# Performance work log

Hardware: AMD Instinct MI355X
Metric: run time of the kernel (lower is better)

Reference implementation:

```python
import jax, jax.numpy as jnp
import numpy as np

LOG_MAX = float(np.log(1000.0 / 16.0))  # dw/dh clamp from BoxCoder.decode
NMS_THRESH = 0.7


def setup_inputs() -> dict:
    key = jax.random.key(0)
    k1, k2, k3, k4, k5, k6 = jax.random.split(key, 6)
    N, B = 262144, 4
    im_h, im_w = 800, 1280
    # plausible anchors: random centers inside image, sizes in [16, 216]
    cx = jax.random.uniform(k1, (N,)) * im_w
    cy = jax.random.uniform(k2, (N,)) * im_h
    aw = jax.random.uniform(k3, (N,)) * 200.0 + 16.0
    ah = jax.random.uniform(k4, (N,)) * 200.0 + 16.0
    anchors = jnp.stack([cx - 0.5 * aw, cy - 0.5 * ah, cx + 0.5 * aw, cy + 0.5 * ah], axis=1).astype(jnp.float32)
    pred_bbox_deltas = (jax.random.normal(k5, (B, N, 4)) * 0.2).astype(jnp.float32)
    objectness = jax.random.normal(k6, (B, N)).astype(jnp.float32)
    return {
        'anchors': anchors,
        'pred_bbox_deltas': pred_bbox_deltas,
        'objectness': objectness,
        'im_h': im_h,
        'im_w': im_w,
        'post_nms_top_n': 1000,
    }


def _decode_clip(anchors, deltas, im_h, im_w):
    # BoxCoder.decode with weights (1,1,1,1), then clip to image bounds.
    aw = anchors[:, 2] - anchors[:, 0]          # [N]
    ah = anchors[:, 3] - anchors[:, 1]
    acx = anchors[:, 0] + 0.5 * aw
    acy = anchors[:, 1] + 0.5 * ah
    dx, dy = deltas[..., 0], deltas[..., 1]     # [B,N]
    dw = jnp.minimum(deltas[..., 2], LOG_MAX)
    dh = jnp.minimum(deltas[..., 3], LOG_MAX)
    pcx = dx * aw + acx
    pcy = dy * ah + acy
    pw = jnp.exp(dw) * aw
    ph = jnp.exp(dh) * ah
    x1 = jnp.clip(pcx - 0.5 * pw, 0.0, im_w)
    y1 = jnp.clip(pcy - 0.5 * ph, 0.0, im_h)
    x2 = jnp.clip(pcx + 0.5 * pw, 0.0, im_w)
    y2 = jnp.clip(pcy + 0.5 * ph, 0.0, im_h)
    return jnp.stack([x1, y1, x2, y2], axis=-1)  # [B,N,4]


def _nms_indices(boxes, scores, k):
    # Greedy NMS (torchvision semantics: suppress IoU > thresh), fixed k picks.
    bs = jax.lax.stop_gradient(boxes)           # indices are non-differentiable
    ss = jax.lax.stop_gradient(scores)
    areas = (bs[:, 2] - bs[:, 0]) * (bs[:, 3] - bs[:, 1])

    def body(cur, _):
        i = jnp.argmax(cur)
        picked = cur[i]
        bb = bs[i]
        ix1 = jnp.maximum(bb[0], bs[:, 0])
        iy1 = jnp.maximum(bb[1], bs[:, 1])
        ix2 = jnp.minimum(bb[2], bs[:, 2])
        iy2 = jnp.minimum(bb[3], bs[:, 3])
        inter = jnp.maximum(ix2 - ix1, 0.0) * jnp.maximum(iy2 - iy1, 0.0)
        barea = (bb[2] - bb[0]) * (bb[3] - bb[1])
        iou = inter / (barea + areas - inter + 1e-9)
        cur = jnp.where(iou > NMS_THRESH, -jnp.inf, cur).at[i].set(-jnp.inf)
        return cur, (i, picked)

    _, (idx, picked) = jax.lax.scan(body, ss, None, length=k)
    return idx, jnp.isfinite(picked)            # valid flags pad positions


def reference(anchors, pred_bbox_deltas, objectness, im_h, im_w, post_nms_top_n):
    boxes = _decode_clip(anchors, pred_bbox_deltas, float(im_h), float(im_w))  # [B,N,4]
    area = (boxes[..., 2] - boxes[..., 0]) * (boxes[..., 3] - boxes[..., 1])
    # area > 1 filter, expressed as score masking (keeps shapes static)
    scores = jnp.where(area > 1.0, objectness, -jnp.inf)

    idx, valid = jax.vmap(lambda b, s: _nms_indices(b, s, post_nms_top_n))(boxes, scores)
    kept_boxes = jnp.take_along_axis(boxes, idx[..., None], axis=1)   # [B,K,4]
    kept_scores = jnp.take_along_axis(scores, idx, axis=1)            # [B,K]
    vf = valid.astype(boxes.dtype)
    kept_boxes = kept_boxes * vf[..., None]
    kept_scores = jnp.where(valid, kept_scores, 0.0)
    # [B, K, 6] = (x1,y1,x2,y2,score,valid)
    return jnp.concatenate([kept_boxes, kept_scores[..., None], vf[..., None]], axis=-1)
```

## Files before the change

### kernel.cpp

```cpp
#include <hip/hip_runtime.h>
#include <cstdint>
#include <cstddef>

#define NBINS 32768
#define FINB 64u
#define CAP_C 2048
#define NW (CAP_C / 64)
#define WP (NW + 1)
#define TARGET 1792u
#define KMAX 1008
#define MROWS 16
#define HB 1024
#define HE 32768
#define CNT_STRIDE 64
#define CPB 64

typedef unsigned long long u64;

__device__ __forceinline__ unsigned orderable(float f) {
  unsigned b = __float_as_uint(f);
  return (b & 0x80000000u) ? ~b : (b | 0x80000000u);
}

__global__ void decode_kernel(const float4* __restrict__ anchors,
                              const float4* __restrict__ deltas,
                              const float* __restrict__ obj,
                              const int* __restrict__ im_h_p,
                              const int* __restrict__ im_w_p,
                              float4* __restrict__ boxes,
                              unsigned* __restrict__ keys,
                              unsigned* __restrict__ hist,
                              int N, int B) {
#pragma clang fp contract(off)
  int n = blockIdx.x * blockDim.x + threadIdx.x;
  int stride = gridDim.x * blockDim.x;
  for (int j = n; j < B * NBINS; j += stride) hist[j] = 0u;
  if (n >= N) return;
  float imw = (float)(*im_w_p);
  float imh = (float)(*im_h_p);
  float4 a = anchors[n];
  float aw = a.z - a.x;
  float ah = a.w - a.y;
  float acx = a.x + 0.5f * aw;
  float acy = a.y + 0.5f * ah;
  const float LOGM = 4.135166556742356f;
  for (int b = 0; b < B; ++b) {
    size_t off = (size_t)b * N + n;
    float4 d = deltas[off];
    float dw = fminf(d.z, LOGM), dh = fminf(d.w, LOGM);
    float pcx = d.x * aw + acx;
    float pcy = d.y * ah + acy;
    float pw = expf(dw) * aw;
    float ph = expf(dh) * ah;
    float x1 = fminf(fmaxf(pcx - 0.5f * pw, 0.0f), imw);
    float y1 = fminf(fmaxf(pcy - 0.5f * ph, 0.0f), imh);
    float x2 = fminf(fmaxf(pcx + 0.5f * pw, 0.0f), imw);
    float y2 = fminf(fmaxf(pcy + 0.5f * ph, 0.0f), imh);
    boxes[off] = make_float4(x1, y1, x2, y2);
    float area = (x2 - x1) * (y2 - y1);
    float sc = (area > 1.0f) ? obj[off] : -__builtin_inff();
    keys[off] = orderable(sc);
  }
}

__global__ void __launch_bounds__(HB) hist_kernel(const unsigned* __restrict__ keys,
                                                  unsigned* __restrict__ hist,
                                                  int N) {
  __shared__ unsigned hl[NBINS / 2];
  int t = threadIdx.x, b = blockIdx.y;
  for (int i = t; i < NBINS / 2; i += HB) hl[i] = 0u;
  __syncthreads();
  const uint4* kb = (const uint4*)(keys + (size_t)b * N) + (size_t)blockIdx.x * (HE / 4);
  int lim = HE / 4;
  int rem4 = (N - blockIdx.x * HE) / 4;
  if (lim > rem4) lim = rem4;
  for (int i = t; i < lim; i += HB) {
    uint4 v = kb[i];
    unsigned b0 = v.x >> 17, b1 = v.y >> 17, b2 = v.z >> 17, b3 = v.w >> 17;
    atomicAdd(&hl[b0 >> 1], (b0 & 1u) ? 65536u : 1u);
    atomicAdd(&hl[b1 >> 1], (b1 & 1u) ? 65536u : 1u);
    atomicAdd(&hl[b2 >> 1], (b2 & 1u) ? 65536u : 1u);
    atomicAdd(&hl[b3 >> 1], (b3 & 1u) ? 65536u : 1u);
  }
  __syncthreads();
  unsigned* hg = hist + (size_t)b * NBINS;
  for (int i = t; i < NBINS / 2; i += HB) {
    unsigned v = hl[i];
    unsigned clo = v & 0xFFFFu, chi = v >> 16;
    if (clo) atomicAdd(&hg[2 * i], clo);
    if (chi) atomicAdd(&hg[2 * i + 1], chi);
  }
}

__global__ void __launch_bounds__(1024) threshold_kernel(const unsigned* __restrict__ hist,
                                                         unsigned* __restrict__ T_lo,
                                                         unsigned* __restrict__ cnt) {
  const int BPT = NBINS / 1024;
  __shared__ unsigned s_part[1024];
  __shared__ unsigned s_T;
  int b = blockIdx.x, t = threadIdx.x;
  const unsigned* h = hist + (size_t)b * NBINS;
  if (t == 0) { s_T = 0xFFFFFFFFu; cnt[b * CNT_STRIDE] = 0u; }
  unsigned mysum = 0;
  const uint4* h4 = (const uint4*)(h + t * BPT);
  for (int k = 0; k < BPT / 4; ++k) {
    int bin0 = t * BPT + k * 4;
    if (bin0 >= (int)FINB) {
      uint4 v = h4[k];
      mysum += v.x + v.y + v.z + v.w;
    }
  }
  s_part[t] = mysum;
  __syncthreads();
  for (int d = 1; d < 1024; d <<= 1) {
    unsigned v = (t + d < 1024) ? s_part[t + d] : 0u;
    __syncthreads();
    s_part[t] += v;
    __syncthreads();
  }
  unsigned total = s_part[0];
  unsigned target = (TARGET < total) ? TARGET : total;
  unsigned above = (t + 1 < 1024) ? s_part[t + 1] : 0u;
  if (total > 0u && above < target && s_part[t] >= target) {
    unsigned c = above;
    for (int k = BPT - 1; k >= 0; --k) {
      unsigned bin = (unsigned)(t * BPT + k);
      if (bin < FINB) break;
      unsigned hv = h[bin];
      c += hv;
      if (c >= target) {
        unsigned T = bin;
        if (c > CAP_C && (c - hv) > 0u) T = bin + 1u;
        s_T = T;
        break;
      }
    }
  }
  __syncthreads();
  if (t == 0) T_lo[b] = (total == 0u) ? 0xFFFFFFFFu : s_T;
}

__global__ void __launch_bounds__(1024) compact_kernel(const unsigned* __restrict__ keys,
                                                       const unsigned* __restrict__ T_lo,
                                                       u64* __restrict__ cand,
                                                       unsigned* __restrict__ cnt, int N) {
  __shared__ u64 s_w[4096];
  __shared__ unsigned s_n, s_base;
  int b = blockIdx.y, t = threadIdx.x;
  if (t == 0) s_n = 0u;
  __syncthreads();
  unsigned T = T_lo[b];
  int slice4 = N / 4 / CPB;
  const uint4* k4 = (const uint4*)(keys + (size_t)b * N) + (size_t)blockIdx.x * slice4;
  for (int i = t; i < slice4; i += 1024) {
    uint4 v = k4[i];
    int bi = (blockIdx.x * slice4 + i) * 4;
    if ((v.x >> 17) >= T) { unsigned p = atomicAdd(&s_n, 1u); if (p < 4096u) s_w[p] = ((u64)v.x << 32) | (unsigned)(~(bi + 0)); }
    if ((v.y >> 17) >= T) { unsigned p = atomicAdd(&s_n, 1u); if (p < 4096u) s_w[p] = ((u64)v.y << 32) | (unsigned)(~(bi + 1)); }
    if ((v.z >> 17) >= T) { unsigned p = atomicAdd(&s_n, 1u); if (p < 4096u) s_w[p] = ((u64)v.z << 32) | (unsigned)(~(bi + 2)); }
    if ((v.w >> 17) >= T) { unsigned p = atomicAdd(&s_n, 1u); if (p < 4096u) s_w[p] = ((u64)v.w << 32) | (unsigned)(~(bi + 3)); }
  }
  __syncthreads();
  unsigned n = s_n < 4096u ? s_n : 4096u;
  if (t == 0) s_base = (n > 0u) ? atomicAdd(&cnt[b * CNT_STRIDE], n) : 0u;
  __syncthreads();
  unsigned gb = s_base;
  for (unsigned j = t; j < n; j += 1024) {
    unsigned p = gb + j;
    if (p < CAP_C) cand[(size_t)b * CAP_C + p] = s_w[j];
  }
}

__global__ void __launch_bounds__(1024) sort_kernel(const u64* __restrict__ cand,
                                                    const unsigned* __restrict__ cntp,
                                                    const float4* __restrict__ boxes,
                                                    float4* __restrict__ sboxes,
                                                    float* __restrict__ sscore,
                                                    int N) {
  __shared__ u64 sk[CAP_C];
  int b = blockIdx.x, t = threadIdx.x;
  int cnt = (int)cntp[b * CNT_STRIDE];
  if (cnt > CAP_C) cnt = CAP_C;
  for (int i = t; i < CAP_C; i += 1024)
    sk[i] = (i < cnt) ? cand[(size_t)b * CAP_C + i] : 0ull;
  __syncthreads();
  for (unsigned kk = 2; kk <= CAP_C; kk <<= 1) {
    for (unsigned j = kk >> 1; j >= 1u; j >>= 1) {
      if (j >= 64u) __syncthreads();
      unsigned pid = (unsigned)t;
      unsigned i = ((pid & ~(j - 1u)) << 1) | (pid & (j - 1u));
      unsigned p = i | j;
      u64 va = sk[i], vb = sk[p];
      bool up = ((i & kk) == 0u);
      bool sw = up ? (va < vb) : (va > vb);
      if (sw) { sk[i] = vb; sk[p] = va; }
    }
  }
  __syncthreads();
  for (int i = t; i < CAP_C; i += 1024) {
    u64 key = sk[i];
    float4 bx = make_float4(0.f, 0.f, 0.f, 0.f);
    float sc = -__builtin_inff();
    if (i < cnt) {
      unsigned idx = ~(unsigned)(key & 0xFFFFFFFFull);
      bx = boxes[(size_t)b * N + idx];
      unsigned u = (unsigned)(key >> 32);
      unsigned sb2 = (u & 0x80000000u) ? (u ^ 0x80000000u) : ~u;
      sc = __uint_as_float(sb2);
    }
    sboxes[(size_t)b * CAP_C + i] = bx;
    sscore[(size_t)b * CAP_C + i] = sc;
  }
}

__global__ void __launch_bounds__(256) mask_kernel(const float4* __restrict__ sboxes,
                                                   u64* __restrict__ mask) {
#pragma clang fp contract(off)
  __shared__ float4 sb[CAP_C];
  int b = blockIdx.y, t = threadIdx.x;
  int wave = t >> 6, lane = t & 63;
  const float4* src = sboxes + (size_t)b * CAP_C;
  for (int i = t; i < CAP_C; i += 256) sb[i] = src[i];
  __syncthreads();
  for (int r = 0; r < MROWS; ++r) {
    int row = blockIdx.x * MROWS + r;
    float4 rb = sb[row];
    float ra = (rb.z - rb.x) * (rb.w - rb.y);
    for (int chunk = wave; chunk < NW; chunk += 4) {
      float4 cb = sb[chunk * 64 + lane];
      float ix1 = fmaxf(rb.x, cb.x), iy1 = fmaxf(rb.y, cb.y);
      float ix2 = fminf(rb.z, cb.z), iy2 = fminf(rb.w, cb.w);
      float inter = fmaxf(ix2 - ix1, 0.0f) * fmaxf(iy2 - iy1, 0.0f);
      float ca = (cb.z - cb.x) * (cb.w - cb.y);
      float iou = inter / (ra + ca - inter + 1e-9f);
      u64 bal = __ballot(iou > 0.7f);
      if (lane == 0)
        mask[((size_t)b * CAP_C + row) * NW + chunk] = bal;
    }
  }
}

__global__ void __launch_bounds__(256, 1) walk_kernel(const u64* __restrict__ mask,
                                                      const float4* __restrict__ sboxes,
                                                      const float* __restrict__ sscore,
                                                      const unsigned* __restrict__ cntp,
                                                      float* __restrict__ out, int K) {
  __shared__ u64 s_buf[2][64 * WP];
  __shared__ int s_keep[KMAX];
  __shared__ int s_ctl[4];
  const int b = blockIdx.x;
  const int t = threadIdx.x;
  const int wave = t >> 6, lane = t & 63;
  const u64* M = mask + (size_t)b * CAP_C * NW;
  int cnt = (int)cntp[b * CNT_STRIDE];
  if (cnt > CAP_C) cnt = CAP_C;
  const u64 lane_above = (lane == 63) ? 0ull : (~0ull << (lane + 1));

  for (int k = 0; k < 8; ++k) {
    int e = k * 256 + t;
    s_buf[0][(e >> 5) * WP + (e & 31)] = M[e];
  }
  if (t == 0) { s_ctl[0] = 0; s_ctl[1] = 0; s_ctl[2] = 0; }
  __syncthreads();

  u64 removed = 0ull;
  int nk = 0;
  int base = 0;
  int cur = 0;

  for (int tt = 0; tt < CAP_C / 64; ++tt) {
    int par = tt & 1;
    if (wave != 0) {
      int nt = base + 64;
      if (nt > CAP_C - 64) nt = CAP_C - 64;
      const u64* src = M + (size_t)nt * NW;
      u64* dst = s_buf[cur ^ 1];
      int s = t - 64;
      for (int k = 0; k < 11; ++k) {
        int e = k * 192 + s;
        if (e < 64 * NW)
          dst[(e >> 5) * WP + (e & 31)] = src[e];
      }
    } else {
      const u64* buf = s_buf[cur];
      int tw = base >> 6;
      u64 D = buf[(size_t)lane * WP + tw];
      unsigned rlo = __builtin_amdgcn_readlane((unsigned)(removed & 0xFFFFFFFFull), tw);
      unsigned rhi = __builtin_amdgcn_readlane((unsigned)(removed >> 32), tw);
      u64 in_rm = ((u64)rhi << 32) | (u64)rlo;
      int rem = cnt - base;
      u64 valid = (rem >= 64) ? ~0ull : ((rem <= 0) ? 0ull : ((1ull << rem) - 1ull));
      u64 pend = (~in_rm) & valid;
      u64 keep = 0ull;
      while (pend != 0ull) {
        bool cond = ((pend >> lane) & 1ull) && ((D & pend & lane_above) != 0ull);
        u64 bal = __ballot((int)cond);
        if (bal == 0ull) { keep |= pend; break; }
        int f = __builtin_ctzll(bal);
        u64 beq = (2ull << f) - 1ull;
        keep |= pend & beq;
        unsigned dlo = __builtin_amdgcn_readlane((unsigned)(D & 0xFFFFFFFFull), f);
        unsigned dhi = __builtin_amdgcn_readlane((unsigned)(D >> 32), f);
        u64 rowf = ((u64)dhi << 32) | (u64)dlo;
        pend &= ~beq;
        pend &= ~rowf;
      }
      int cap = K - nk;
      int kc = __popcll(keep);
      if (kc > cap) {
        bool mine = ((keep >> lane) & 1ull) &&
                    (__popcll(keep & ((1ull << lane) - 1ull)) < cap);
        keep = __ballot((int)mine);
        kc = cap;
      }
      if ((keep >> lane) & 1ull)
        s_keep[nk + __popcll(keep & ((1ull << lane) - 1ull))] = base + lane;
      nk += kc;
      int lw = lane & 31;
      u64 ac0 = 0, ac1 = 0, ac2 = 0, ac3 = 0;
#pragma unroll
      for (int r = 0; r < 64; r += 4) {
        u64 m0 = buf[(size_t)(r + 0) * WP + lw];
        u64 m1 = buf[(size_t)(r + 1) * WP + lw];
        u64 m2 = buf[(size_t)(r + 2) * WP + lw];
        u64 m3 = buf[(size_t)(r + 3) * WP + lw];
        ac0 |= m0 & ((u64)0 - ((keep >> (r + 0)) & 1ull));
        ac1 |= m1 & ((u64)0 - ((keep >> (r + 1)) & 1ull));
        ac2 |= m2 & ((u64)0 - ((keep >> (r + 2)) & 1ull));
        ac3 |= m3 & ((u64)0 - ((keep >> (r + 3)) & 1ull));
      }
      removed |= (ac0 | ac1) | (ac2 | ac3);
      int stop = (base + 64 >= cnt) || (nk >= K);
      if (lane == 0) { s_ctl[par] = stop; s_ctl[2] = nk; }
    }
    __syncthreads();
    if (s_ctl[par]) break;
    base += 64;
    cur ^= 1;
  }
  __syncthreads();
  int nkf = s_ctl[2];
  for (int j = t; j < nkf; j += 256) {
    int i = s_keep[j];
    float4 bx = sboxes[(size_t)b * CAP_C + i];
    float sc = sscore[(size_t)b * CAP_C + i];
    float* row = out + ((size_t)b * K + j) * 6;
    row[0] = bx.x; row[1] = bx.y; row[2] = bx.z; row[3] = bx.w;
    row[4] = sc; row[5] = 1.0f;
  }
  for (int j = nkf + t; j < K; j += 256) {
    float* row = out + ((size_t)b * K + j) * 6;
    row[0] = 0.f; row[1] = 0.f; row[2] = 0.f; row[3] = 0.f;
    row[4] = 0.f; row[5] = 0.f;
  }
}

extern "C" void kernel_launch(void* const* d_in, const int* in_sizes, int n_in,
                              void* d_out, int out_size, void* d_ws, size_t ws_size,
                              hipStream_t stream) {
  const float4* anchors = (const float4*)d_in[0];
  const float4* deltas = (const float4*)d_in[1];
  const float* obj = (const float*)d_in[2];
  const int* imh = (const int*)d_in[3];
  const int* imw = (const int*)d_in[4];
  int N = in_sizes[0] / 4;
  int B = in_sizes[2] / N;
  int K = out_size / (B * 6);
  if (K > KMAX) K = KMAX;

  char* ws = (char*)d_ws;
  size_t off = 0;
  float4* boxes = (float4*)(ws + off);            off += (size_t)B * N * 16;
  float4* sboxes = (float4*)(ws + off);           off += (size_t)B * CAP_C * 16;
  u64* cand = (u64*)(ws + off);                   off += (size_t)B * CAP_C * 8;
  u64* mask = (u64*)(ws + off);                   off += (size_t)B * CAP_C * NW * 8;
  unsigned* keys = (unsigned*)(ws + off);         off += (size_t)B * N * 4;
  unsigned* hist = (unsigned*)(ws + off);         off += (size_t)B * NBINS * 4;
  float* sscore = (float*)(ws + off);             off += (size_t)B * CAP_C * 4;
  unsigned* T_lo = (unsigned*)(ws + off);         off += (size_t)B * 4;
  off = (off + 255) & ~(size_t)255;
  unsigned* cnt = (unsigned*)(ws + off);          off += (size_t)B * CNT_STRIDE * 4;
  float* out = (float*)d_out;

  int nb = (N + 255) / 256;
  int P = (N + HE - 1) / HE;
  decode_kernel<<<nb, 256, 0, stream>>>(anchors, deltas, obj, imh, imw,
                                        boxes, keys, hist, N, B);
  hist_kernel<<<dim3(P, B), HB, 0, stream>>>(keys, hist, N);
  threshold_kernel<<<B, 1024, 0, stream>>>(hist, T_lo, cnt);
  compact_kernel<<<dim3(CPB, B), 1024, 0, stream>>>(keys, T_lo, cand, cnt, N);
  sort_kernel<<<B, 1024, 0, stream>>>(cand, cnt, boxes, sboxes, sscore, N);
  mask_kernel<<<dim3(CAP_C / MROWS, B), 256, 0, stream>>>(sboxes, mask);
  walk_kernel<<<B, 256, 0, stream>>>(mask, sboxes, sscore, cnt, out, K);
}
```

Baseline: 170.9 us.

## Drop full box buffer, fuse threshold into histogram, skip lower-triangle mask work

Decode no longer writes the full B×N box array; the sort kernel recomputes boxes only for the selected candidates from anchors and deltas. The threshold pass is merged into the histogram kernel, with the last-arriving block per batch doing the scan, which removes one launch. The mask kernel skips chunks below the diagonal, and the walk kernel reorganizes its removed-mask accumulation into vectorized 128-bit loads plus shuffle reductions with padded rows. These cut global memory writes, launches and redundant IoU work, at the cost of recomputing exp for candidates and relying on an atomic arrival counter.

New measurement: 184.9 us. 1.08x slower.

```diff
diff --git a/kernel.cpp b/kernel.cpp
--- a/kernel.cpp
+++ b/kernel.cpp
@@ -6,13 +6,14 @@
 #define FINB 64u
 #define CAP_C 2048
 #define NW (CAP_C / 64)
-#define WP (NW + 1)
+#define WP (NW + 2)
 #define TARGET 1792u
 #define KMAX 1008
 #define MROWS 16
 #define HB 1024
 #define HE 32768
 #define CNT_STRIDE 64
+#define ARRIVE_OFF 16
 #define CPB 64
 
 typedef unsigned long long u64;
@@ -20,6 +21,12 @@
 __device__ __forceinline__ unsigned orderable(float f) {
   unsigned b = __float_as_uint(f);
   return (b & 0x80000000u) ? ~b : (b | 0x80000000u);
+}
+
+__device__ __forceinline__ u64 shfl_xor_u64(u64 v, int m) {
+  int lo = __shfl_xor((int)(unsigned)(v & 0xFFFFFFFFull), m, 64);
+  int hi = __shfl_xor((int)(unsigned)(v >> 32), m, 64);
+  return ((u64)(unsigned)hi << 32) | (u64)(unsigned)lo;
 }
 
 __global__ void decode_kernel(const float4* __restrict__ anchors,
@@ -27,14 +34,15 @@
                               const float* __restrict__ obj,
                               const int* __restrict__ im_h_p,
                               const int* __restrict__ im_w_p,
-                              float4* __restrict__ boxes,
                               unsigned* __restrict__ keys,
                               unsigned* __restrict__ hist,
+                              unsigned* __restrict__ cnt,
                               int N, int B) {
 #pragma clang fp contract(off)
   int n = blockIdx.x * blockDim.x + threadIdx.x;
   int stride = gridDim.x * blockDim.x;
   for (int j = n; j < B * NBINS; j += stride) hist[j] = 0u;
+  for (int j = n; j < B * CNT_STRIDE; j += stride) cnt[j] = 0u;
   if (n >= N) return;
   float imw = (float)(*im_w_p);
   float imh = (float)(*im_h_p);
@@ -56,7 +64,6 @@
     float y1 = fminf(fmaxf(pcy - 0.5f * ph, 0.0f), imh);
     float x2 = fminf(fmaxf(pcx + 0.5f * pw, 0.0f), imw);
     float y2 = fminf(fmaxf(pcy + 0.5f * ph, 0.0f), imh);
-    boxes[off] = make_float4(x1, y1, x2, y2);
     float area = (x2 - x1) * (y2 - y1);
     float sc = (area > 1.0f) ? obj[off] : -__builtin_inff();
     keys[off] = orderable(sc);
@@ -65,6 +72,8 @@
 
 __global__ void __launch_bounds__(HB) hist_kernel(const unsigned* __restrict__ keys,
                                                   unsigned* __restrict__ hist,
+                                                  unsigned* __restrict__ T_lo,
+                                                  unsigned* __restrict__ cnt,
                                                   int N) {
   __shared__ unsigned hl[NBINS / 2];
   int t = threadIdx.x, b = blockIdx.y;
@@ -90,54 +99,50 @@
     if (clo) atomicAdd(&hg[2 * i], clo);
     if (chi) atomicAdd(&hg[2 * i + 1], chi);
   }
-}
-
-__global__ void __launch_bounds__(1024) threshold_kernel(const unsigned* __restrict__ hist,
-                                                         unsigned* __restrict__ T_lo,
-                                                         unsigned* __restrict__ cnt) {
+  __syncthreads();
+  if (t == 0) {
+    __threadfence();
+    unsigned old = atomicAdd(&cnt[b * CNT_STRIDE + ARRIVE_OFF], 1u);
+    hl[4096] = (old == gridDim.x - 1u) ? 1u : 0u;
+  }
+  __syncthreads();
+  if (hl[4096] == 0u) return;
   const int BPT = NBINS / 1024;
-  __shared__ unsigned s_part[1024];
-  __shared__ unsigned s_T;
-  int b = blockIdx.x, t = threadIdx.x;
-  const unsigned* h = hist + (size_t)b * NBINS;
-  if (t == 0) { s_T = 0xFFFFFFFFu; cnt[b * CNT_STRIDE] = 0u; }
   unsigned mysum = 0;
-  const uint4* h4 = (const uint4*)(h + t * BPT);
-  for (int k = 0; k < BPT / 4; ++k) {
-    int bin0 = t * BPT + k * 4;
-    if (bin0 >= (int)FINB) {
-      uint4 v = h4[k];
-      mysum += v.x + v.y + v.z + v.w;
-    }
-  }
-  s_part[t] = mysum;
+  for (int k = 0; k < BPT; ++k) {
+    unsigned bin = (unsigned)(t * BPT + k);
+    if (bin >= FINB)
+      mysum += __hip_atomic_load(&hg[bin], __ATOMIC_RELAXED, __HIP_MEMORY_SCOPE_AGENT);
+  }
+  if (t == 0) hl[2048] = 0xFFFFFFFFu;
+  hl[t] = mysum;
   __syncthreads();
   for (int d = 1; d < 1024; d <<= 1) {
-    unsigned v = (t + d < 1024) ? s_part[t + d] : 0u;
+    unsigned v = (t + d < 1024) ? hl[t + d] : 0u;
     __syncthreads();
-    s_part[t] += v;
+    hl[t] += v;
     __syncthreads();
   }
-  unsigned total = s_part[0];
+  unsigned total = hl[0];
   unsigned target = (TARGET < total) ? TARGET : total;
-  unsigned above = (t + 1 < 1024) ? s_part[t + 1] : 0u;
-  if (total > 0u && above < target && s_part[t] >= target) {
+  unsigned above = (t + 1 < 1024) ? hl[t + 1] : 0u;
+  if (total > 0u && above < target && hl[t] >= target) {
     unsigned c = above;
     for (int k = BPT - 1; k >= 0; --k) {
       unsigned bin = (unsigned)(t * BPT + k);
       if (bin < FINB) break;
-      unsigned hv = h[bin];
+      unsigned hv = __hip_atomic_load(&hg[bin], __ATOMIC_RELAXED, __HIP_MEMORY_SCOPE_AGENT);
       c += hv;
       if (c >= target) {
         unsigned T = bin;
         if (c > CAP_C && (c - hv) > 0u) T = bin + 1u;
-        s_T = T;
+        hl[2048] = T;
         break;
       }
     }
   }
   __syncthreads();
-  if (t == 0) T_lo[b] = (total == 0u) ? 0xFFFFFFFFu : s_T;
+  if (t == 0) T_lo[b] = (total == 0u) ? 0xFFFFFFFFu : hl[2048];
 }
 
 __global__ void __launch_bounds__(1024) compact_kernel(const unsigned* __restrict__ keys,
@@ -173,10 +178,14 @@
 
 __global__ void __launch_bounds__(1024) sort_kernel(const u64* __restrict__ cand,
                                                     const unsigned* __restrict__ cntp,
-                                                    const float4* __restrict__ boxes,
+                                                    const float4* __restrict__ anchors,
+                                                    const float4* __restrict__ deltas,
+                                                    const int* __restrict__ im_h_p,
+                                                    const int* __restrict__ im_w_p,
                                                     float4* __restrict__ sboxes,
                                                     float* __restrict__ sscore,
                                                     int N) {
+#pragma clang fp contract(off)
   __shared__ u64 sk[CAP_C];
   int b = blockIdx.x, t = threadIdx.x;
   int cnt = (int)cntp[b * CNT_STRIDE];
@@ -197,13 +206,30 @@
     }
   }
   __syncthreads();
+  float imw = (float)(*im_w_p);
+  float imh = (float)(*im_h_p);
+  const float LOGM = 4.135166556742356f;
   for (int i = t; i < CAP_C; i += 1024) {
     u64 key = sk[i];
     float4 bx = make_float4(0.f, 0.f, 0.f, 0.f);
     float sc = -__builtin_inff();
     if (i < cnt) {
       unsigned idx = ~(unsigned)(key & 0xFFFFFFFFull);
-      bx = boxes[(size_t)b * N + idx];
+      float4 a = anchors[idx];
+      float4 d = deltas[(size_t)b * N + idx];
+      float aw = a.z - a.x;
+      float ah = a.w - a.y;
+      float acx = a.x + 0.5f * aw;
+      float acy = a.y + 0.5f * ah;
+      float dw = fminf(d.z, LOGM), dh = fminf(d.w, LOGM);
+      float pcx = d.x * aw + acx;
+      float pcy = d.y * ah + acy;
+      float pw = expf(dw) * aw;
+      float ph = expf(dh) * ah;
+      bx.x = fminf(fmaxf(pcx - 0.5f * pw, 0.0f), imw);
+      bx.y = fminf(fmaxf(pcy - 0.5f * ph, 0.0f), imh);
+      bx.z = fminf(fmaxf(pcx + 0.5f * pw, 0.0f), imw);
+      bx.w = fminf(fmaxf(pcy + 0.5f * ph, 0.0f), imh);
       unsigned u = (unsigned)(key >> 32);
       unsigned sb2 = (u & 0x80000000u) ? (u ^ 0x80000000u) : ~u;
       sc = __uint_as_float(sb2);
@@ -224,9 +250,11 @@
   __syncthreads();
   for (int r = 0; r < MROWS; ++r) {
     int row = blockIdx.x * MROWS + r;
+    int c0 = row >> 6;
     float4 rb = sb[row];
     float ra = (rb.z - rb.x) * (rb.w - rb.y);
     for (int chunk = wave; chunk < NW; chunk += 4) {
+      if (chunk < c0) continue;
       float4 cb = sb[chunk * 64 + lane];
       float ix1 = fmaxf(rb.x, cb.x), iy1 = fmaxf(rb.y, cb.y);
       float ix2 = fminf(rb.z, cb.z), iy2 = fminf(rb.w, cb.w);
@@ -263,10 +291,12 @@
   if (t == 0) { s_ctl[0] = 0; s_ctl[1] = 0; s_ctl[2] = 0; }
   __syncthreads();
 
-  u64 removed = 0ull;
+  u64 rm0 = 0ull, rm1 = 0ull;
   int nk = 0;
   int base = 0;
   int cur = 0;
+  const int pr = (lane & 15) * 2;
+  const int grp = lane >> 4;
 
   for (int tt = 0; tt < CAP_C / 64; ++tt) {
     int par = tt & 1;
@@ -285,8 +315,9 @@
       const u64* buf = s_buf[cur];
       int tw = base >> 6;
       u64 D = buf[(size_t)lane * WP + tw];
-      unsigned rlo = __builtin_amdgcn_readlane((unsigned)(removed & 0xFFFFFFFFull), tw);
-      unsigned rhi = __builtin_amdgcn_readlane((unsigned)(removed >> 32), tw);
+      u64 rmw = (tw & 1) ? rm1 : rm0;
+      unsigned rlo = __builtin_amdgcn_readlane((unsigned)(rmw & 0xFFFFFFFFull), tw >> 1);
+      unsigned rhi = __builtin_amdgcn_readlane((unsigned)(rmw >> 32), tw >> 1);
       u64 in_rm = ((u64)rhi << 32) | (u64)rlo;
       int rem = cnt - base;
       u64 valid = (rem >= 64) ? ~0ull : ((rem <= 0) ? 0ull : ((1ull << rem) - 1ull));
@@ -316,20 +347,21 @@
       if ((keep >> lane) & 1ull)
         s_keep[nk + __popcll(keep & ((1ull << lane) - 1ull))] = base + lane;
       nk += kc;
-      int lw = lane & 31;
-      u64 ac0 = 0, ac1 = 0, ac2 = 0, ac3 = 0;
+      u64 a0 = 0ull, a1 = 0ull;
 #pragma unroll
-      for (int r = 0; r < 64; r += 4) {
-        u64 m0 = buf[(size_t)(r + 0) * WP + lw];
-        u64 m1 = buf[(size_t)(r + 1) * WP + lw];
-        u64 m2 = buf[(size_t)(r + 2) * WP + lw];
-        u64 m3 = buf[(size_t)(r + 3) * WP + lw];
-        ac0 |= m0 & ((u64)0 - ((keep >> (r + 0)) & 1ull));
-        ac1 |= m1 & ((u64)0 - ((keep >> (r + 1)) & 1ull));
-        ac2 |= m2 & ((u64)0 - ((keep >> (r + 2)) & 1ull));
-        ac3 |= m3 & ((u64)0 - ((keep >> (r + 3)) & 1ull));
+      for (int rr = 0; rr < 16; ++rr) {
+        int r = grp * 16 + rr;
+        ulonglong2 v = *(const ulonglong2*)&buf[(size_t)r * WP + pr];
+        u64 m = (u64)0 - ((keep >> r) & 1ull);
+        a0 |= v.x & m;
+        a1 |= v.y & m;
       }
-      removed |= (ac0 | ac1) | (ac2 | ac3);
+      a0 |= shfl_xor_u64(a0, 16);
+      a0 |= shfl_xor_u64(a0, 32);
+      a1 |= shfl_xor_u64(a1, 16);
+      a1 |= shfl_xor_u64(a1, 32);
+      rm0 |= a0;
+      rm1 |= a1;
       int stop = (base + 64 >= cnt) || (nk >= K);
       if (lane == 0) { s_ctl[par] = stop; s_ctl[2] = nk; }
     }
@@ -370,10 +402,9 @@
 
   char* ws = (char*)d_ws;
   size_t off = 0;
-  float4* boxes = (float4*)(ws + off);            off += (size_t)B * N * 16;
   float4* sboxes = (float4*)(ws + off);           off += (size_t)B * CAP_C * 16;
+  u64* mask = (u64*)(ws + off);                   off += (size_t)B * CAP_C * NW * 8;
   u64* cand = (u64*)(ws + off);                   off += (size_t)B * CAP_C * 8;
-  u64* mask = (u64*)(ws + off);                   off += (size_t)B * CAP_C * NW * 8;
   unsigned* keys = (unsigned*)(ws + off);         off += (size_t)B * N * 4;
   unsigned* hist = (unsigned*)(ws + off);         off += (size_t)B * NBINS * 4;
   float* sscore = (float*)(ws + off);             off += (size_t)B * CAP_C * 4;
@@ -385,11 +416,11 @@
   int nb = (N + 255) / 256;
   int P = (N + HE - 1) / HE;
   decode_kernel<<<nb, 256, 0, stream>>>(anchors, deltas, obj, imh, imw,
-                                        boxes, keys, hist, N, B);
-  hist_kernel<<<dim3(P, B), HB, 0, stream>>>(keys, hist, N);
-  threshold_kernel<<<B, 1024, 0, stream>>>(hist, T_lo, cnt);
+                                        keys, hist, cnt, N, B);
+  hist_kernel<<<dim3(P, B), HB, 0, stream>>>(keys, hist, T_lo, cnt, N);
   compact_kernel<<<dim3(CPB, B), 1024, 0, stream>>>(keys, T_lo, cand, cnt, N);
-  sort_kernel<<<B, 1024, 0, stream>>>(cand, cnt, boxes, sboxes, sscore, N);
+  sort_kernel<<<B, 1024, 0, stream>>>(cand, cnt, anchors, deltas, imh, imw,
+                                      sboxes, sscore, N);
   mask_kernel<<<dim3(CAP_C / MROWS, B), 256, 0, stream>>>(sboxes, mask);
   walk_kernel<<<B, 256, 0, stream>>>(mask, sboxes, sscore, cnt, out, K);
 }
```
